# Optimization experiments

Hardware: AMD Instinct MI355X
Metric: run time of the kernel (lower is better)

Reference implementation:

```python
import jax, jax.numpy as jnp
import numpy as np

# ActivationWithGain: activation scaled so a standard-normal input keeps unit variance.
_s = np.random.default_rng(0).standard_normal(1 << 20).astype(np.float32)
GAIN = float(1.0 / (_s / (1.0 + np.exp(-_s))).std())  # SiLU gain ~ 1.787
INV_SQRT2 = np.float32(1.0 / np.sqrt(2.0))


def _act(x):
    return jax.nn.silu(x) * jnp.float32(GAIN)


def setup_inputs() -> dict:
    key = jax.random.key(0)
    ks = jax.random.split(key, 9)
    n_up, n_dn, n_nuc, dim, edim = 512, 512, 256, 256, 32
    n_el = n_up + n_dn
    n_edges = n_el * n_nuc  # dense electron-nucleus bipartite graph
    return {
        "elec_emb": jax.random.normal(ks[0], (n_el, dim), jnp.float32),
        "up_inp": jax.random.normal(ks[1], (n_nuc, dim), jnp.float32),
        "down_inp": jax.random.normal(ks[2], (n_nuc, dim), jnp.float32),
        "edge_emb": jax.random.normal(ks[3], (n_edges, edim), jnp.float32),
        "contr": jax.random.uniform(ks[4], (n_edges,), jnp.float32),
        "norm": jax.random.uniform(ks[5], (n_el,), jnp.float32),
        "W_out": jax.random.normal(ks[6], (dim, dim), jnp.float32) / np.float32(np.sqrt(dim)),
        "b_out": jnp.zeros((dim,), jnp.float32),
        "W_edge": jax.random.normal(ks[7], (edim, dim), jnp.float32) / np.float32(np.sqrt(edim)),
        "W_out2": jax.random.normal(ks[8], (dim, dim), jnp.float32) / np.float32(np.sqrt(dim)),
        "b_out2": jnp.zeros((dim,), jnp.float32),
        "scale1": jnp.ones((), jnp.float32),  # FixedScalingFactor (frozen after init)
        "scale2": jnp.ones((), jnp.float32),
        "n_up": n_up,
        "n_down": n_dn,
        "n_nuclei": n_nuc,
    }


def reference(elec_emb, up_inp, down_inp, edge_emb, contr, norm,
              W_out, b_out, W_edge, W_out2, b_out2, scale1, scale2,
              n_up, n_down, n_nuclei):
    n_el = n_up + n_down
    # adj_idx for a single graph: dense bipartite edges, sorted by electron index
    e_n_i = jnp.repeat(jnp.arange(n_el), n_nuclei)   # [E] electron index per edge
    e_n_k = jnp.tile(jnp.arange(n_nuclei), n_el)     # [E] nucleus index per edge

    out_emb = elec_emb @ W_out + b_out               # Dense(out_dim)

    mask = jnp.arange(n_el) < n_up                   # spin_mask: True for spin-up electrons
    e_n_mask = mask[e_n_i]
    # gather nuclear embeddings per edge, selecting up/down table by electron spin
    inp = jnp.where(e_n_mask[:, None], up_inp[e_n_k], down_inp[e_n_k])  # [E, D]

    weights = edge_emb @ W_edge                      # Dense_no_bias(out_dim), [E, D]
    # FixedScalingFactor: contr only weights the init-time variance estimate;
    # at runtime the op is x * scale1.
    to_elec = inp * weights * scale1                 # [E, D]

    agg = jax.ops.segment_sum(to_elec, e_n_i, num_segments=n_el,
                              indices_are_sorted=True)  # [n_el, D]
    out_emb = (out_emb + agg * norm[:, None]) * scale2
    out_emb = _act(out_emb)
    out_emb = _act(out_emb @ W_out2 + b_out2)
    # residual: shapes match, so rescaled sum
    return (elec_emb + out_emb) * INV_SQRT2
```

## Files before the change

kernel.cpp:

```cpp
#include <hip/hip_runtime.h>
#include <hip/hip_bf16.h>

#define N_EL   1024
#define N_UP   512
#define NNUC   256
#define DIM    256
#define EDIM   32
#define KTOT   8192
#define NKP    8

#define GAIN_F      1.7872135f
#define INV_SQRT2_F 0.7071067811865476f

typedef __attribute__((ext_vector_type(8))) short bf16x8;
typedef __attribute__((ext_vector_type(4))) short bf16x4;
typedef __attribute__((ext_vector_type(4))) float f32x4;

__device__ __forceinline__ short f2bf(float x) {
    union { __hip_bfloat16 h; short s; } u;
    u.h = __float2bfloat16(x);
    return u.s;
}

__global__ __launch_bounds__(256) void prep_kernel(
    const float* __restrict__ up, const float* __restrict__ dn,
    const float* __restrict__ wedge,
    const float* __restrict__ w1, const float* __restrict__ w2,
    const float* __restrict__ elec, const float* __restrict__ eemb,
    short* __restrict__ w1f, short* __restrict__ w2f,
    short* __restrict__ elecb, short* __restrict__ Tf,
    short* __restrict__ eembb)
{
    const int idx = (blockIdx.x << 8) + threadIdx.x;

    if (idx < 65536) {
        {
            const int b  = idx & 7;
            const int l  = (idx >> 3) & 63;
            const int q  = (idx >> 9) & 7;
            const int nt = idx >> 12;
            const int j  = (q << 5) + ((l >> 4) << 3) + b;
            const int d  = (nt << 4) + (l & 15);
            w1f[idx] = f2bf(w1[j * DIM + d]);
            w2f[idx] = f2bf(w2[j * DIM + d]);
        }
        {
            const f32x4 v = *(const f32x4*)(elec + (idx << 2));
            bf16x4 o;
            o[0] = f2bf(v[0]); o[1] = f2bf(v[1]);
            o[2] = f2bf(v[2]); o[3] = f2bf(v[3]);
            *(bf16x4*)(elecb + (idx << 2)) = o;
        }
    }

    if (idx < 524288) {
        const int s   = idx >> 18;
        const int rem = idx & 262143;
        const int kt  = rem >> 10;
        const int dt  = (rem >> 6) & 15;
        const int l   = rem & 63;
        const int d   = (dt << 4) + (l & 15);
        const int jb  = (l >> 4) << 3;
        const float* __restrict__ inp = s ? dn : up;
        const float iv = inp[kt * DIM + d];
        const float* __restrict__ wcol = wedge + d;
        bf16x8 o;
        #pragma unroll
        for (int b = 0; b < 8; ++b)
            o[b] = f2bf(iv * wcol[(jb + b) * DIM]);
        *(bf16x8*)(Tf + ((size_t)s << 21) + ((size_t)rem << 3)) = o;
    }

    {
        const int mt16 = idx >> 14;
        const int kt   = (idx >> 6) & 255;
        const int l    = idx & 63;
        const int row  = (mt16 << 4) + (l & 15);
        const int kk   = (kt << 5) + ((l >> 4) << 3);
        const float* src = eemb + (size_t)row * KTOT + kk;
        const f32x4 lo = *(const f32x4*)src;
        const f32x4 hi = *(const f32x4*)(src + 4);
        bf16x8 o;
        o[0] = f2bf(lo[0]); o[1] = f2bf(lo[1]);
        o[2] = f2bf(lo[2]); o[3] = f2bf(lo[3]);
        o[4] = f2bf(hi[0]); o[5] = f2bf(hi[1]);
        o[6] = f2bf(hi[2]); o[7] = f2bf(hi[3]);
        *(bf16x8*)(eembb + ((size_t)idx << 3)) = o;
    }
}

__global__ __launch_bounds__(512) void edge_gemm(
    const short* __restrict__ eembb,
    const short* __restrict__ Tf,
    float* __restrict__ P)
{
    const int tid  = threadIdx.x;
    const int w    = tid >> 6;
    const int lane = tid & 63;
    const int g    = lane >> 4;
    const int c    = lane & 15;
    const int kp   = blockIdx.x & 7;
    const int rt   = blockIdx.x >> 3;
    const int rb   = rt << 5;

    const short* __restrict__ Tb = Tf + ((rb < N_UP) ? 0 : (1 << 21));

    auto LOADA = [&](int sub, bf16x8 (&ad)[2][4]) {
        #pragma unroll
        for (int rr = 0; rr < 2; ++rr) {
            const int mt16 = (rt << 1) + rr;
            #pragma unroll
            for (int q = 0; q < 4; ++q) {
                const int kt = (kp << 5) + (sub << 2) + q;
                ad[rr][q] = *(const bf16x8*)(
                    eembb + ((size_t)(((mt16 << 8) + kt) << 6) + lane) * 8);
            }
        }
    };
    auto LOADB = [&](int sub, bf16x8 (&bd)[8]) {
        #pragma unroll
        for (int t = 0; t < 2; ++t) {
            const int ct = (w << 1) + t;
            #pragma unroll
            for (int q = 0; q < 4; ++q) {
                const int ktg = (kp << 5) + (sub << 2) + q;
                bd[(t << 2) + q] = *(const bf16x8*)(
                    Tb + (((((ktg << 4) + ct) << 6) + lane) << 3));
            }
        }
    };

    f32x4 acc[2][2] = {{{0.f,0.f,0.f,0.f},{0.f,0.f,0.f,0.f}},
                       {{0.f,0.f,0.f,0.f},{0.f,0.f,0.f,0.f}}};

    auto COMPUTE = [&](bf16x8 (&a)[2][4], bf16x8 (&bc)[8]) {
        #pragma unroll
        for (int q = 0; q < 4; ++q) {
            acc[0][0] = __builtin_amdgcn_mfma_f32_16x16x32_bf16(a[0][q], bc[q],     acc[0][0], 0, 0, 0);
            acc[0][1] = __builtin_amdgcn_mfma_f32_16x16x32_bf16(a[0][q], bc[4 + q], acc[0][1], 0, 0, 0);
            acc[1][0] = __builtin_amdgcn_mfma_f32_16x16x32_bf16(a[1][q], bc[q],     acc[1][0], 0, 0, 0);
            acc[1][1] = __builtin_amdgcn_mfma_f32_16x16x32_bf16(a[1][q], bc[4 + q], acc[1][1], 0, 0, 0);
        }
    };

    bf16x8 aA[2][4], aB[2][4], bA[8], bB[8];

    LOADA(0, aA);
    LOADB(0, bA);

    #pragma unroll
    for (int sub = 0; sub < 8; ++sub) {
        if ((sub & 1) == 0) {
            if (sub < 7) { LOADA(sub + 1, aB); LOADB(sub + 1, bB); }
            COMPUTE(aA, bA);
        } else {
            if (sub < 7) { LOADA(sub + 1, aA); LOADB(sub + 1, bA); }
            COMPUTE(aB, bB);
        }
    }

    float* __restrict__ Pp = P + ((size_t)kp << 18);
    #pragma unroll
    for (int rr = 0; rr < 2; ++rr)
        #pragma unroll
        for (int t = 0; t < 2; ++t) {
            const int ct = (w << 1) + t;
            #pragma unroll
            for (int j = 0; j < 4; ++j) {
                const int row = rb + (rr << 4) + (g << 2) + j;
                Pp[(row << 8) + (ct << 4) + c] = acc[rr][t][j];
            }
        }
}

__global__ __launch_bounds__(256) void reduce_kernel(
    const float* __restrict__ P,
    const float* __restrict__ s1p,
    float* __restrict__ agg)
{
    const int idx = (blockIdx.x << 8) + threadIdx.x;
    const float s1 = *s1p;
    f32x4 s = {0.f, 0.f, 0.f, 0.f};
    #pragma unroll
    for (int kp = 0; kp < NKP; ++kp) {
        const f32x4 v = *(const f32x4*)(P + ((size_t)kp << 18) + (idx << 2));
        s[0] += v[0]; s[1] += v[1]; s[2] += v[2]; s[3] += v[3];
    }
    s[0] *= s1; s[1] *= s1; s[2] *= s1; s[3] *= s1;
    *(f32x4*)(agg + (idx << 2)) = s;
}

__global__ __launch_bounds__(512) void out_kernel(
    const short* __restrict__ elecb,
    const short* __restrict__ w1f, const short* __restrict__ w2f,
    const float* __restrict__ elec, const float* __restrict__ agg,
    const float* __restrict__ norm,
    const float* __restrict__ b1, const float* __restrict__ b2,
    const float* __restrict__ s2p,
    float* __restrict__ outp)
{
    __shared__ short h_s[16][264];

    const int tid  = threadIdx.x;
    const int w    = tid >> 6;
    const int lane = tid & 63;
    const int g    = lane >> 4;
    const int c    = lane & 15;
    const int mt   = blockIdx.x >> 2;
    const int qd   = blockIdx.x & 3;
    const int mb   = mt << 4;

    const short* abase = elecb + ((mb + c) << 8) + (g << 3);
    bf16x8 a[8];
    #pragma unroll
    for (int q = 0; q < 8; ++q) a[q] = *(const bf16x8*)(abase + (q << 5));

    const float s2 = *s2p;

    #pragma unroll
    for (int t = 0; t < 2; ++t) {
        const int ct = (w << 1) + t;
        const short* bb = w1f + (ct << 12) + (lane << 3);
        bf16x8 b[8];
        #pragma unroll
        for (int q = 0; q < 8; ++q) b[q] = *(const bf16x8*)(bb + (q << 9));
        f32x4 acc = {0.f, 0.f, 0.f, 0.f};
        #pragma unroll
        for (int q = 0; q < 8; ++q)
            acc = __builtin_amdgcn_mfma_f32_16x16x32_bf16(a[q], b[q], acc, 0, 0, 0);

        const int n  = (ct << 4) + c;
        const float bv = b1[n];
        #pragma unroll
        for (int r = 0; r < 4; ++r) {
            const int mr = (g << 2) + r;
            const int m  = mb + mr;
            const float y = (acc[r] + bv + agg[(m << 8) + n] * norm[m]) * s2;
            const float sig = 1.f / (1.f + __expf(-y));
            h_s[mr][n] = f2bf(GAIN_F * y * sig);
        }
    }
    __syncthreads();

    if (w < 4) {
        bf16x8 a2[8];
        #pragma unroll
        for (int q = 0; q < 8; ++q)
            a2[q] = *(const bf16x8*)(&h_s[c][(q << 5) + (g << 3)]);

        const int ct = (qd << 2) + w;
        const short* bb = w2f + (ct << 12) + (lane << 3);
        bf16x8 b[8];
        #pragma unroll
        for (int q = 0; q < 8; ++q) b[q] = *(const bf16x8*)(bb + (q << 9));
        f32x4 acc = {0.f, 0.f, 0.f, 0.f};
        #pragma unroll
        for (int q = 0; q < 8; ++q)
            acc = __builtin_amdgcn_mfma_f32_16x16x32_bf16(a2[q], b[q], acc, 0, 0, 0);

        const int n  = (ct << 4) + c;
        const float bv = b2[n];
        #pragma unroll
        for (int r = 0; r < 4; ++r) {
            const int m = mb + (g << 2) + r;
            const float z = acc[r] + bv;
            const float sig = 1.f / (1.f + __expf(-z));
            const float o = GAIN_F * z * sig;
            outp[(m << 8) + n] = (elec[(m << 8) + n] + o) * INV_SQRT2_F;
        }
    }
}

extern "C" void kernel_launch(void* const* d_in, const int* in_sizes, int n_in,
                              void* d_out, int out_size, void* d_ws, size_t ws_size,
                              hipStream_t stream)
{
    const float* elec  = (const float*)d_in[0];
    const float* up    = (const float*)d_in[1];
    const float* dn    = (const float*)d_in[2];
    const float* eemb  = (const float*)d_in[3];
    const float* norm  = (const float*)d_in[5];
    const float* W1    = (const float*)d_in[6];
    const float* b1    = (const float*)d_in[7];
    const float* Wedge = (const float*)d_in[8];
    const float* W2    = (const float*)d_in[9];
    const float* b2    = (const float*)d_in[10];
    const float* s1    = (const float*)d_in[11];
    const float* s2    = (const float*)d_in[12];

    short* sbase = (short*)d_ws;
    short* w1f   = sbase;
    short* w2f   = sbase + 65536;
    short* elecb = sbase + 131072;
    short* Tf    = sbase + 393216;
    short* eembb = sbase + 393216 + 4194304;
    float* P     = (float*)(sbase + 393216 + 4194304 + 8388608);
    float* agg   = P + (size_t)NKP * 262144;

    prep_kernel  <<<4096, 256, 0, stream>>>(up, dn, Wedge, W1, W2, elec, eemb,
                                            w1f, w2f, elecb, Tf, eembb);
    edge_gemm    <<<256, 512, 0, stream>>>(eembb, Tf, P);
    reduce_kernel<<<256, 256, 0, stream>>>(P, s1, agg);
    out_kernel   <<<256, 512, 0, stream>>>(elecb, w1f, w2f, elec, agg, norm,
                                           b1, b2, s2, (float*)d_out);
}
```

Baseline: 35.37 us.

## Build edge-weight B operand on the fly inside edge GEMM instead of materializing it

The bf16 tensor T (up/down nuclear input times W_edge), previously written to global memory by the prep kernel and read back by the edge GEMM, is now formed in registers. The GEMM keeps W_edge slices in registers, loads fp32 nuclear inputs per k-step, and multiplies and converts them to bf16 fragments right before the MFMAs. This removes an 8 MB write and its re-read, at the cost of extra VALU multiply and convert work and more registers in the GEMM inner loop.

Result: slower. 37.40 us (+5.8%).

```diff
diff --git a/kernel.cpp b/kernel.cpp
--- a/kernel.cpp
+++ b/kernel.cpp
@@ -23,13 +23,10 @@
 }
 
 __global__ __launch_bounds__(256) void prep_kernel(
-    const float* __restrict__ up, const float* __restrict__ dn,
-    const float* __restrict__ wedge,
     const float* __restrict__ w1, const float* __restrict__ w2,
     const float* __restrict__ elec, const float* __restrict__ eemb,
     short* __restrict__ w1f, short* __restrict__ w2f,
-    short* __restrict__ elecb, short* __restrict__ Tf,
-    short* __restrict__ eembb)
+    short* __restrict__ elecb, short* __restrict__ eembb)
 {
     const int idx = (blockIdx.x << 8) + threadIdx.x;
 
@@ -51,24 +48,6 @@
             o[2] = f2bf(v[2]); o[3] = f2bf(v[3]);
             *(bf16x4*)(elecb + (idx << 2)) = o;
         }
-    }
-
-    if (idx < 524288) {
-        const int s   = idx >> 18;
-        const int rem = idx & 262143;
-        const int kt  = rem >> 10;
-        const int dt  = (rem >> 6) & 15;
-        const int l   = rem & 63;
-        const int d   = (dt << 4) + (l & 15);
-        const int jb  = (l >> 4) << 3;
-        const float* __restrict__ inp = s ? dn : up;
-        const float iv = inp[kt * DIM + d];
-        const float* __restrict__ wcol = wedge + d;
-        bf16x8 o;
-        #pragma unroll
-        for (int b = 0; b < 8; ++b)
-            o[b] = f2bf(iv * wcol[(jb + b) * DIM]);
-        *(bf16x8*)(Tf + ((size_t)s << 21) + ((size_t)rem << 3)) = o;
     }
 
     {
@@ -91,7 +70,8 @@
 
 __global__ __launch_bounds__(512) void edge_gemm(
     const short* __restrict__ eembb,
-    const short* __restrict__ Tf,
+    const float* __restrict__ up, const float* __restrict__ dn,
+    const float* __restrict__ wedge,
     float* __restrict__ P)
 {
     const int tid  = threadIdx.x;
@@ -103,7 +83,16 @@
     const int rt   = blockIdx.x >> 3;
     const int rb   = rt << 5;
 
-    const short* __restrict__ Tb = Tf + ((rb < N_UP) ? 0 : (1 << 21));
+    const float* __restrict__ inp = (rb < N_UP) ? up : dn;
+    const int d0 = ((w << 1) << 4) + c;
+    const int d1 = d0 + 16;
+
+    float wf0[8], wf1[8];
+    #pragma unroll
+    for (int b = 0; b < 8; ++b) {
+        wf0[b] = wedge[((g << 3) + b) * DIM + d0];
+        wf1[b] = wedge[((g << 3) + b) * DIM + d1];
+    }
 
     auto LOADA = [&](int sub, bf16x8 (&ad)[2][4]) {
         #pragma unroll
@@ -117,16 +106,25 @@
             }
         }
     };
-    auto LOADB = [&](int sub, bf16x8 (&bd)[8]) {
-        #pragma unroll
-        for (int t = 0; t < 2; ++t) {
-            const int ct = (w << 1) + t;
+    auto LOADI = [&](int sub, float (&iv)[4][2]) {
+        const int k0 = (kp << 5) + (sub << 2);
+        #pragma unroll
+        for (int q = 0; q < 4; ++q) {
+            iv[q][0] = inp[((k0 + q) << 8) + d0];
+            iv[q][1] = inp[((k0 + q) << 8) + d1];
+        }
+    };
+    auto MAKEB = [&](float (&iv)[4][2], bf16x8 (&bd)[8]) {
+        #pragma unroll
+        for (int q = 0; q < 4; ++q) {
+            union { bf16x8 v; short s[8]; } f0, f1;
             #pragma unroll
-            for (int q = 0; q < 4; ++q) {
-                const int ktg = (kp << 5) + (sub << 2) + q;
-                bd[(t << 2) + q] = *(const bf16x8*)(
-                    Tb + (((((ktg << 4) + ct) << 6) + lane) << 3));
+            for (int b = 0; b < 8; ++b) {
+                f0.s[b] = f2bf(wf0[b] * iv[q][0]);
+                f1.s[b] = f2bf(wf1[b] * iv[q][1]);
             }
+            bd[q]     = f0.v;
+            bd[4 + q] = f1.v;
         }
     };
 
@@ -143,19 +141,23 @@
         }
     };
 
-    bf16x8 aA[2][4], aB[2][4], bA[8], bB[8];
+    bf16x8 aA[2][4], aB[2][4];
+    float  ivA[4][2], ivB[4][2];
 
     LOADA(0, aA);
-    LOADB(0, bA);
+    LOADI(0, ivA);
 
     #pragma unroll
     for (int sub = 0; sub < 8; ++sub) {
+        bf16x8 bc[8];
         if ((sub & 1) == 0) {
-            if (sub < 7) { LOADA(sub + 1, aB); LOADB(sub + 1, bB); }
-            COMPUTE(aA, bA);
+            if (sub < 7) { LOADA(sub + 1, aB); LOADI(sub + 1, ivB); }
+            MAKEB(ivA, bc);
+            COMPUTE(aA, bc);
         } else {
-            if (sub < 7) { LOADA(sub + 1, aA); LOADB(sub + 1, bA); }
-            COMPUTE(aB, bB);
+            if (sub < 7) { LOADA(sub + 1, aA); LOADI(sub + 1, ivA); }
+            MAKEB(ivB, bc);
+            COMPUTE(aB, bc);
         }
     }
 
@@ -292,14 +294,13 @@
     short* w1f   = sbase;
     short* w2f   = sbase + 65536;
     short* elecb = sbase + 131072;
-    short* Tf    = sbase + 393216;
-    short* eembb = sbase + 393216 + 4194304;
-    float* P     = (float*)(sbase + 393216 + 4194304 + 8388608);
+    short* eembb = sbase + 393216;
+    float* P     = (float*)(sbase + 393216 + 8388608);
     float* agg   = P + (size_t)NKP * 262144;
 
-    prep_kernel  <<<4096, 256, 0, stream>>>(up, dn, Wedge, W1, W2, elec, eemb,
-                                            w1f, w2f, elecb, Tf, eembb);
-    edge_gemm    <<<256, 512, 0, stream>>>(eembb, Tf, P);
+    prep_kernel  <<<4096, 256, 0, stream>>>(W1, W2, elec, eemb,
+                                            w1f, w2f, elecb, eembb);
+    edge_gemm    <<<256, 512, 0, stream>>>(eembb, up, dn, Wedge, P);
     reduce_kernel<<<256, 256, 0, stream>>>(P, s1, agg);
     out_kernel   <<<256, 512, 0, stream>>>(elecb, w1f, w2f, elec, agg, norm,
                                            b1, b2, s2, (float*)d_out);
```
